# Performance work log

Hardware: AMD Instinct MI355X
Metric: run time of the kernel (lower is better)

## Reference

```python
import jax, jax.numpy as jnp
import numpy as np

NUM_NODES = 80000
NUM_EDGES = 1280000
NUM_GRAPHS = 512
IN_DIM = 64
HID = 64
NUM_CLASSES = 10


def setup_inputs() -> dict:
    key = jax.random.key(0)
    ks = jax.random.split(key, 16)
    x = jax.random.normal(ks[0], (NUM_NODES, IN_DIM), dtype=jnp.float32)
    edge_index = jax.random.randint(ks[1], (2, NUM_EDGES), 0, NUM_NODES, dtype=jnp.int64)
    batch = jnp.sort(jax.random.randint(ks[2], (NUM_NODES,), 0, NUM_GRAPHS, dtype=jnp.int64))

    def glorot(k, shape):
        fan_in, fan_out = shape[1], shape[0]
        lim = jnp.sqrt(6.0 / (fan_in + fan_out))
        return jax.random.uniform(k, shape, dtype=jnp.float32, minval=-lim, maxval=lim)

    inp = {
        "x": x,
        "edge_index": edge_index,
        "batch": batch,
        # GraphConv layer 1: lin_rel (with bias) applied to aggregated neighbors, lin_root (no bias)
        "w_rel1": glorot(ks[3], (HID, IN_DIM)),
        "b_rel1": jnp.zeros((HID,), dtype=jnp.float32),
        "w_root1": glorot(ks[4], (HID, IN_DIM)),
        # layer 2
        "w_rel2": glorot(ks[5], (HID, HID)),
        "b_rel2": jnp.zeros((HID,), dtype=jnp.float32),
        "w_root2": glorot(ks[6], (HID, HID)),
        # layer 3
        "w_rel3": glorot(ks[7], (HID, HID)),
        "b_rel3": jnp.zeros((HID,), dtype=jnp.float32),
        "w_root3": glorot(ks[8], (HID, HID)),
        # final linear head
        "w_lin": glorot(ks[9], (NUM_CLASSES, HID)),
        "b_lin": jnp.zeros((NUM_CLASSES,), dtype=jnp.float32),
    }
    return inp


def _graph_conv(x, src, dst, w_rel, b_rel, w_root):
    # PyG GraphConv with aggr='add': out_i = W_rel @ (sum_{j in N(i)} x_j) + b_rel + W_root @ x_i
    agg = jax.ops.segment_sum(x[src], dst, num_segments=NUM_NODES)  # [N, d_in]
    return agg @ w_rel.T + b_rel + x @ w_root.T


def reference(x, edge_index, batch,
              w_rel1, b_rel1, w_root1,
              w_rel2, b_rel2, w_root2,
              w_rel3, b_rel3, w_root3,
              w_lin, b_lin):
    src, dst = edge_index[0], edge_index[1]
    h = jax.nn.relu(_graph_conv(x, src, dst, w_rel1, b_rel1, w_root1))
    h = jax.nn.relu(_graph_conv(h, src, dst, w_rel2, b_rel2, w_root2))
    h = _graph_conv(h, src, dst, w_rel3, b_rel3, w_root3)
    # global_mean_pool over graph ids
    sums = jax.ops.segment_sum(h, batch, num_segments=NUM_GRAPHS)          # [G, HID]
    counts = jax.ops.segment_sum(jnp.ones((h.shape[0],), h.dtype), batch, num_segments=NUM_GRAPHS)
    pooled = sums / jnp.maximum(counts, 1.0)[:, None]
    # dropout p=0.5 is identity at inference (training=False)
    return pooled @ w_lin.T + b_lin  # [G, NUM_CLASSES]
```

## Files before the change

kernel.cpp:

```cpp
#include <hip/hip_runtime.h>

#define N_NODES  80000
#define N_EDGES  1280000
#define N_GRAPHS 512
#define DIM      64
#define NCLS     10

#define ETILE    8192
#define NTILE    157
#define NCB      157
#define CBPAD    160

typedef short short8f __attribute__((ext_vector_type(8)));
typedef float float4f __attribute__((ext_vector_type(4)));

static __device__ __forceinline__ unsigned short f2bf(float f) {
    unsigned u = __float_as_uint(f);
    unsigned r = (u + 0x7FFFu + ((u >> 16) & 1u)) >> 16;
    return (unsigned short)r;
}
static __device__ __forceinline__ float bf_lo(unsigned v) { return __uint_as_float(v << 16); }
static __device__ __forceinline__ float bf_hi(unsigned v) { return __uint_as_float(v & 0xFFFF0000u); }

__global__ __launch_bounds__(256) void k_hist(const int* __restrict__ ei,
                                              int* __restrict__ hmat) {
    __shared__ int hist[NCB];
    int tile = blockIdx.x, t = threadIdx.x;
    for (int i = t; i < NCB; i += 256) hist[i] = 0;
    __syncthreads();
    int base = tile * ETILE;
    int end = base + ETILE; if (end > N_EDGES) end = N_EDGES;
    for (int i = base + t; i < end; i += 256)
        atomicAdd(&hist[ei[N_EDGES + i] >> 9], 1);
    __syncthreads();
    for (int i = t; i < NCB; i += 256) hmat[tile * CBPAD + i] = hist[i];
}

__global__ __launch_bounds__(256) void k_scanT(const int* __restrict__ hmat,
        int* __restrict__ obase, int* __restrict__ btot) {
    __shared__ int sa[256], sb[256];
    int b = blockIdx.x, t = threadIdx.x;
    int v = (t < NTILE) ? hmat[t * CBPAD + b] : 0;
    sa[t] = v; __syncthreads();
    int* sp = sa; int* dp = sb;
    for (int off = 1; off < 256; off <<= 1) {
        dp[t] = sp[t] + ((t >= off) ? sp[t - off] : 0);
        __syncthreads();
        int* tmp = sp; sp = dp; dp = tmp;
    }
    int incl = sp[t];
    if (t < NTILE) obase[t * CBPAD + b] = incl - v;
    if (t == NTILE - 1) btot[b] = incl;
}

__global__ __launch_bounds__(256) void k_scanB(const int* __restrict__ btot,
        int* __restrict__ bucketbase, int* __restrict__ rowptr) {
    __shared__ int sa[256], sb[256];
    int t = threadIdx.x;
    int v = (t < NCB) ? btot[t] : 0;
    sa[t] = v; __syncthreads();
    int* sp = sa; int* dp = sb;
    for (int off = 1; off < 256; off <<= 1) {
        dp[t] = sp[t] + ((t >= off) ? sp[t - off] : 0);
        __syncthreads();
        int* tmp = sp; sp = dp; dp = tmp;
    }
    int incl = sp[t];
    if (t < NCB) bucketbase[t] = incl - v;
    if (t == 0) { bucketbase[NCB] = N_EDGES; rowptr[N_NODES] = N_EDGES; }
}

__global__ __launch_bounds__(256) void k_scatter(const int* __restrict__ ei,
        const int* __restrict__ obase, const int* __restrict__ bucketbase,
        int* __restrict__ ebuf) {
    __shared__ int cur[NCB];
    int tile = blockIdx.x, t = threadIdx.x;
    for (int i = t; i < NCB; i += 256)
        cur[i] = bucketbase[i] + obase[tile * CBPAD + i];
    __syncthreads();
    int base = tile * ETILE;
    int end = base + ETILE; if (end > N_EDGES) end = N_EDGES;
    for (int i = base + t; i < end; i += 256) {
        int s = ei[i], d = ei[N_EDGES + i];
        int p = atomicAdd(&cur[d >> 9], 1);
        ebuf[p] = s | ((d & 511) << 17);
    }
}

__global__ __launch_bounds__(256) void k_csr(const int* __restrict__ ebuf,
        const int* __restrict__ bucketbase, int* __restrict__ rowptr,
        int* __restrict__ col) {
    __shared__ int cnt[512];
    __shared__ int sa[512], sb[512];
    __shared__ int cur[512];
    int b = blockIdx.x, t = threadIdx.x;
    int s = bucketbase[b], e = bucketbase[b + 1];
    cnt[t] = 0; cnt[t + 256] = 0;
    __syncthreads();
    for (int i = s + t; i < e; i += 256) atomicAdd(&cnt[ebuf[i] >> 17], 1);
    __syncthreads();
    sa[t] = cnt[t]; sa[t + 256] = cnt[t + 256];
    __syncthreads();
    int* sp = sa; int* dp = sb;
    for (int off = 1; off < 512; off <<= 1) {
        int i1 = t + 256;
        int v0 = sp[t]  + ((t  >= off) ? sp[t  - off] : 0);
        int v1 = sp[i1] + ((i1 >= off) ? sp[i1 - off] : 0);
        __syncthreads();
        dp[t] = v0; dp[i1] = v1;
        __syncthreads();
        int* tmp = sp; sp = dp; dp = tmp;
    }
    int node0 = b * 512;
    int base0 = s + sp[t] - cnt[t];
    int base1 = s + sp[t + 256] - cnt[t + 256];
    cur[t] = base0; cur[t + 256] = base1;
    if (node0 + t < N_NODES)       rowptr[node0 + t] = base0;
    if (node0 + t + 256 < N_NODES) rowptr[node0 + t + 256] = base1;
    __syncthreads();
    for (int i = s + t; i < e; i += 256) {
        int pk = ebuf[i];
        int p = atomicAdd(&cur[pk >> 17], 1);
        col[p] = pk & 0x1FFFF;
    }
}

__global__ __launch_bounds__(256) void k_prep2(const float* __restrict__ x,
        const float* __restrict__ wr1, const float* __restrict__ wo1,
        const float* __restrict__ wr2, const float* __restrict__ wo2,
        unsigned short* __restrict__ xb, unsigned short* __restrict__ wf) {
    int bid = blockIdx.x, t = threadIdx.x;
    if (bid < 5000) {
        int i = bid * 256 + t;
        float4 v = ((const float4*)x)[i];
        ushort4 o;
        o.x = f2bf(v.x); o.y = f2bf(v.y); o.z = f2bf(v.z); o.w = f2bf(v.w);
        ((ushort4*)xb)[i] = o;
    } else {
        int idx = (bid - 5000) * 256 + t;
        int j = idx & 7, lane = (idx >> 3) & 63;
        int ks = (idx >> 9) & 3, nt = (idx >> 11) & 3, l = idx >> 13;
        int k = ks * 32 + ((lane >> 4) & 3) * 8 + j;
        int n = nt * 16 + (lane & 15);
        const float* wr = (l == 0) ? wr1 : wr2;
        const float* wo = (l == 0) ? wo1 : wo2;
        float val = (k < 64) ? wr[n * 64 + k] : wo[n * 64 + (k - 64)];
        wf[idx] = f2bf(val);
    }
}

__global__ __launch_bounds__(256) void k_gather_bf(const unsigned short* __restrict__ Xbf,
        const int* __restrict__ rowptr, const int* __restrict__ col,
        unsigned short* __restrict__ agg) {
    const unsigned* Xu = (const unsigned*)Xbf;
    int t = threadIdx.x, w = t >> 6, lane = t & 63;
    int g = lane >> 5, c = lane & 31;
    int node = blockIdx.x * 8 + w * 2 + g;
    int start = rowptr[node], end = rowptr[node + 1];
    float alo = 0.f, ahi = 0.f;
    int e = start;
    for (; e + 16 <= end; e += 16) {
        unsigned v[16];
#pragma unroll
        for (int j = 0; j < 16; ++j)
            v[j] = Xu[(size_t)col[e + j] * 32 + c];
#pragma unroll
        for (int j = 0; j < 16; ++j) { alo += bf_lo(v[j]); ahi += bf_hi(v[j]); }
    }
    for (; e + 4 <= end; e += 4) {
        unsigned v0 = Xu[(size_t)col[e]     * 32 + c];
        unsigned v1 = Xu[(size_t)col[e + 1] * 32 + c];
        unsigned v2 = Xu[(size_t)col[e + 2] * 32 + c];
        unsigned v3 = Xu[(size_t)col[e + 3] * 32 + c];
        alo += (bf_lo(v0) + bf_lo(v1)) + (bf_lo(v2) + bf_lo(v3));
        ahi += (bf_hi(v0) + bf_hi(v1)) + (bf_hi(v2) + bf_hi(v3));
    }
    for (; e < end; ++e) {
        unsigned v = Xu[(size_t)col[e] * 32 + c];
        alo += bf_lo(v); ahi += bf_hi(v);
    }
    unsigned o = (unsigned)f2bf(alo) | ((unsigned)f2bf(ahi) << 16);
    ((unsigned*)agg)[(size_t)node * 32 + c] = o;
}

__global__ __launch_bounds__(256) void k_linear_mfma(
        const unsigned short* __restrict__ aggb, const unsigned short* __restrict__ xb,
        const unsigned short* __restrict__ wf, const float* __restrict__ bias,
        unsigned short* __restrict__ out, int relu) {
    int t = threadIdx.x, w = t >> 6, lane = t & 63;
    int quad = lane >> 4, l15 = lane & 15;
    int mbase = blockIdx.x * 64 + w * 16;
    size_t arow = (size_t)(mbase + l15) * 64;
    short8f a0 = *(const short8f*)(aggb + arow + quad * 8);
    short8f a1 = *(const short8f*)(aggb + arow + 32 + quad * 8);
    short8f a2 = *(const short8f*)(xb   + arow + quad * 8);
    short8f a3 = *(const short8f*)(xb   + arow + 32 + quad * 8);
    int orow = mbase + quad * 4;
#pragma unroll
    for (int nt = 0; nt < 4; ++nt) {
        const unsigned short* wp = wf + ((size_t)(nt * 4) * 64 + lane) * 8;
        short8f b0 = *(const short8f*)(wp);
        short8f b1 = *(const short8f*)(wp + 64 * 8);
        short8f b2 = *(const short8f*)(wp + 128 * 8);
        short8f b3 = *(const short8f*)(wp + 192 * 8);
        float4f acc = {0.f, 0.f, 0.f, 0.f};
        acc = __builtin_amdgcn_mfma_f32_16x16x32_bf16(a0, b0, acc, 0, 0, 0);
        acc = __builtin_amdgcn_mfma_f32_16x16x32_bf16(a1, b1, acc, 0, 0, 0);
        acc = __builtin_amdgcn_mfma_f32_16x16x32_bf16(a2, b2, acc, 0, 0, 0);
        acc = __builtin_amdgcn_mfma_f32_16x16x32_bf16(a3, b3, acc, 0, 0, 0);
        float bi = bias[nt * 16 + l15];
#pragma unroll
        for (int r = 0; r < 4; ++r) {
            float v = acc[r] + bi;
            if (relu) v = fmaxf(v, 0.f);
            out[(size_t)(orow + r) * 64 + nt * 16 + l15] = f2bf(v);
        }
    }
}

static __device__ __forceinline__ int lowerb(const int* a, int n, int key) {
    int lo = 0, hi = n;
    while (lo < hi) { int mid = (lo + hi) >> 1; if (a[mid] < key) lo = mid + 1; else hi = mid; }
    return lo;
}

__global__ __launch_bounds__(256) void k_gsum(const unsigned short* __restrict__ h2,
        const int* __restrict__ rowptr, const int* __restrict__ col,
        const int* __restrict__ batch, float* __restrict__ S) {
    __shared__ float red1[8][64];
    __shared__ float red2[8][64];
    const unsigned* Xu = (const unsigned*)h2;
    int g = blockIdx.x, t = threadIdx.x;
    int hw = t >> 5, c = t & 31;
    int ns = lowerb(batch, N_NODES, g);
    int ne = lowerb(batch, N_NODES, g + 1);
    int es = rowptr[ns], ee = rowptr[ne];
    float alo = 0.f, ahi = 0.f;
    int nfull = (ee - es) >> 7;
    int e0 = es + hw * 16;
    for (int b = 0; b < nfull; ++b, e0 += 128) {
        unsigned v[16];
#pragma unroll
        for (int j = 0; j < 16; ++j)
            v[j] = Xu[(size_t)col[e0 + j] * 32 + c];
#pragma unroll
        for (int j = 0; j < 16; ++j) { alo += bf_lo(v[j]); ahi += bf_hi(v[j]); }
    }
    for (int e = es + nfull * 128 + hw; e < ee; e += 8) {
        unsigned v = Xu[(size_t)col[e] * 32 + c];
        alo += bf_lo(v); ahi += bf_hi(v);
    }
    float blo = 0.f, bhi = 0.f;
    for (int i = ns + hw; i < ne; i += 8) {
        unsigned v = Xu[(size_t)i * 32 + c];
        blo += bf_lo(v); bhi += bf_hi(v);
    }
    red1[hw][2 * c] = alo; red1[hw][2 * c + 1] = ahi;
    red2[hw][2 * c] = blo; red2[hw][2 * c + 1] = bhi;
    __syncthreads();
    if (t < 64) {
        float v = 0.f;
#pragma unroll
        for (int s = 0; s < 8; ++s) v += red1[s][t];
        S[g * 128 + t] = v;
    } else if (t < 128) {
        float v = 0.f;
#pragma unroll
        for (int s = 0; s < 8; ++s) v += red2[s][t - 64];
        S[g * 128 + 64 + (t - 64)] = v;
    }
}

__global__ __launch_bounds__(64) void k_head2(const float* __restrict__ S,
        const int* __restrict__ batch,
        const float* __restrict__ wr3, const float* __restrict__ wo3,
        const float* __restrict__ b3,
        const float* __restrict__ wlin, const float* __restrict__ blin,
        float* __restrict__ out) {
    __shared__ float s1[64], s2[64], pl[64];
    int g = blockIdx.x, t = threadIdx.x;
    int ns = lowerb(batch, N_NODES, g);
    int ne = lowerb(batch, N_NODES, g + 1);
    float inv = 1.f / (float)((ne > ns) ? (ne - ns) : 1);
    s1[t] = S[g * 128 + t] * inv;
    s2[t] = S[g * 128 + 64 + t] * inv;
    __syncthreads();
    float acc = b3[t];
    for (int k = 0; k < 64; ++k)
        acc += s1[k] * wr3[t * 64 + k] + s2[k] * wo3[t * 64 + k];
    pl[t] = acc;
    __syncthreads();
    float myout = 0.f;
    for (int cls = 0; cls < NCLS; ++cls) {
        float vv = pl[t] * wlin[cls * 64 + t];
        for (int off = 32; off > 0; off >>= 1) vv += __shfl_xor(vv, off);
        if (t == cls) myout = vv + blin[cls];
    }
    if (t < NCLS) out[g * NCLS + t] = myout;
}

extern "C" void kernel_launch(void* const* d_in, const int* in_sizes, int n_in,
                              void* d_out, int out_size, void* d_ws, size_t ws_size,
                              hipStream_t stream) {
    const float* x     = (const float*)d_in[0];
    const int*   ei    = (const int*)d_in[1];
    const int*   batch = (const int*)d_in[2];
    const float* wr1 = (const float*)d_in[3];
    const float* b1  = (const float*)d_in[4];
    const float* wo1 = (const float*)d_in[5];
    const float* wr2 = (const float*)d_in[6];
    const float* b2  = (const float*)d_in[7];
    const float* wo2 = (const float*)d_in[8];
    const float* wr3 = (const float*)d_in[9];
    const float* b3  = (const float*)d_in[10];
    const float* wo3 = (const float*)d_in[11];
    const float* wlin = (const float*)d_in[12];
    const float* blin = (const float*)d_in[13];
    float* out = (float*)d_out;

    char* p = (char*)d_ws;
    auto alloc = [&](size_t bytes) { char* r = p; p += (bytes + 255) & ~(size_t)255; return r; };
    int*   rowptr  = (int*)alloc((N_NODES + 1) * sizeof(int));
    int*   hmat    = (int*)alloc((size_t)NTILE * CBPAD * sizeof(int));
    int*   obase   = (int*)alloc((size_t)NTILE * CBPAD * sizeof(int));
    int*   btot    = (int*)alloc(CBPAD * sizeof(int));
    int*   bucketbase = (int*)alloc((NCB + 1) * sizeof(int));
    int*   ebuf    = (int*)alloc((size_t)N_EDGES * sizeof(int));
    int*   col     = (int*)alloc((size_t)N_EDGES * sizeof(int));
    unsigned short* wf  = (unsigned short*)alloc(2 * 8192 * sizeof(unsigned short));
    unsigned short* xbf = (unsigned short*)alloc((size_t)N_NODES * 64 * 2);
    unsigned short* agg = (unsigned short*)alloc((size_t)N_NODES * 64 * 2);
    unsigned short* hA  = (unsigned short*)alloc((size_t)N_NODES * 64 * 2);
    unsigned short* hB  = (unsigned short*)alloc((size_t)N_NODES * 64 * 2);
    float* S       = (float*)alloc((size_t)N_GRAPHS * 128 * sizeof(float));

    k_hist   <<<NTILE, 256, 0, stream>>>(ei, hmat);
    k_scanT  <<<NCB,   256, 0, stream>>>(hmat, obase, btot);
    k_scanB  <<<1,     256, 0, stream>>>(btot, bucketbase, rowptr);
    k_scatter<<<NTILE, 256, 0, stream>>>(ei, obase, bucketbase, ebuf);
    k_csr    <<<NCB,   256, 0, stream>>>(ebuf, bucketbase, rowptr, col);
    k_prep2  <<<5064,  256, 0, stream>>>(x, wr1, wo1, wr2, wo2, xbf, wf);

    k_gather_bf  <<<N_NODES / 8,  256, 0, stream>>>(xbf, rowptr, col, agg);
    k_linear_mfma<<<N_NODES / 64, 256, 0, stream>>>(agg, xbf, wf,        b1, hA, 1);
    k_gather_bf  <<<N_NODES / 8,  256, 0, stream>>>(hA, rowptr, col, agg);
    k_linear_mfma<<<N_NODES / 64, 256, 0, stream>>>(agg, hA, wf + 8192,  b2, hB, 1);
    k_gsum <<<N_GRAPHS, 256, 0, stream>>>(hB, rowptr, col, batch, S);
    k_head2<<<N_GRAPHS, 64,  0, stream>>>(S, batch, wr3, wo3, b3, wlin, blin, out);
}
```

Before: 279.9 us.

## Gather rows with 16-byte loads across edges and split graph sums four ways

The neighbour gather now has one wavefront per node, with eight lanes per edge each loading 16 bytes, so eight edges are in flight per step. Partial sums are then reduced with cross-lane shuffles, in place of the old scheme where each half-wave streamed all edges with 4-byte loads. The graph-sum kernel splits each graph's node range into four blocks, raising block count for better occupancy, and the head kernel adds the four partials. The cost is extra shuffle work and idle lanes on low-degree nodes.

```diff
diff --git a/kernel.cpp b/kernel.cpp
--- a/kernel.cpp
+++ b/kernel.cpp
@@ -149,38 +149,56 @@
     }
 }
 
-__global__ __launch_bounds__(256) void k_gather_bf(const unsigned short* __restrict__ Xbf,
+__global__ __launch_bounds__(256) void k_gather4(const unsigned short* __restrict__ Xbf,
         const int* __restrict__ rowptr, const int* __restrict__ col,
         unsigned short* __restrict__ agg) {
-    const unsigned* Xu = (const unsigned*)Xbf;
+    const uint4* Xq = (const uint4*)Xbf;
     int t = threadIdx.x, w = t >> 6, lane = t & 63;
-    int g = lane >> 5, c = lane & 31;
-    int node = blockIdx.x * 8 + w * 2 + g;
+    int e = lane >> 3, c = lane & 7;
+    int node = blockIdx.x * 4 + w;
     int start = rowptr[node], end = rowptr[node + 1];
-    float alo = 0.f, ahi = 0.f;
-    int e = start;
-    for (; e + 16 <= end; e += 16) {
-        unsigned v[16];
-#pragma unroll
-        for (int j = 0; j < 16; ++j)
-            v[j] = Xu[(size_t)col[e + j] * 32 + c];
-#pragma unroll
-        for (int j = 0; j < 16; ++j) { alo += bf_lo(v[j]); ahi += bf_hi(v[j]); }
-    }
-    for (; e + 4 <= end; e += 4) {
-        unsigned v0 = Xu[(size_t)col[e]     * 32 + c];
-        unsigned v1 = Xu[(size_t)col[e + 1] * 32 + c];
-        unsigned v2 = Xu[(size_t)col[e + 2] * 32 + c];
-        unsigned v3 = Xu[(size_t)col[e + 3] * 32 + c];
-        alo += (bf_lo(v0) + bf_lo(v1)) + (bf_lo(v2) + bf_lo(v3));
-        ahi += (bf_hi(v0) + bf_hi(v1)) + (bf_hi(v2) + bf_hi(v3));
-    }
-    for (; e < end; ++e) {
-        unsigned v = Xu[(size_t)col[e] * 32 + c];
-        alo += bf_lo(v); ahi += bf_hi(v);
-    }
-    unsigned o = (unsigned)f2bf(alo) | ((unsigned)f2bf(ahi) << 16);
-    ((unsigned*)agg)[(size_t)node * 32 + c] = o;
+    float acc[8] = {0.f, 0.f, 0.f, 0.f, 0.f, 0.f, 0.f, 0.f};
+    int base = start;
+    for (; base + 16 <= end; base += 16) {
+        int i0 = col[base + e];
+        int i1 = col[base + 8 + e];
+        uint4 v0 = Xq[(size_t)i0 * 8 + c];
+        uint4 v1 = Xq[(size_t)i1 * 8 + c];
+        acc[0] += bf_lo(v0.x) + bf_lo(v1.x); acc[1] += bf_hi(v0.x) + bf_hi(v1.x);
+        acc[2] += bf_lo(v0.y) + bf_lo(v1.y); acc[3] += bf_hi(v0.y) + bf_hi(v1.y);
+        acc[4] += bf_lo(v0.z) + bf_lo(v1.z); acc[5] += bf_hi(v0.z) + bf_hi(v1.z);
+        acc[6] += bf_lo(v0.w) + bf_lo(v1.w); acc[7] += bf_hi(v0.w) + bf_hi(v1.w);
+    }
+    for (; base + 8 <= end; base += 8) {
+        int i0 = col[base + e];
+        uint4 v0 = Xq[(size_t)i0 * 8 + c];
+        acc[0] += bf_lo(v0.x); acc[1] += bf_hi(v0.x);
+        acc[2] += bf_lo(v0.y); acc[3] += bf_hi(v0.y);
+        acc[4] += bf_lo(v0.z); acc[5] += bf_hi(v0.z);
+        acc[6] += bf_lo(v0.w); acc[7] += bf_hi(v0.w);
+    }
+    int r = end - base;
+    if (e < r) {
+        int i0 = col[base + e];
+        uint4 v0 = Xq[(size_t)i0 * 8 + c];
+        acc[0] += bf_lo(v0.x); acc[1] += bf_hi(v0.x);
+        acc[2] += bf_lo(v0.y); acc[3] += bf_hi(v0.y);
+        acc[4] += bf_lo(v0.z); acc[5] += bf_hi(v0.z);
+        acc[6] += bf_lo(v0.w); acc[7] += bf_hi(v0.w);
+    }
+#pragma unroll
+    for (int off = 8; off < 64; off <<= 1) {
+#pragma unroll
+        for (int j = 0; j < 8; ++j) acc[j] += __shfl_xor(acc[j], off);
+    }
+    if (e == 0) {
+        uint4 o;
+        o.x = (unsigned)f2bf(acc[0]) | ((unsigned)f2bf(acc[1]) << 16);
+        o.y = (unsigned)f2bf(acc[2]) | ((unsigned)f2bf(acc[3]) << 16);
+        o.z = (unsigned)f2bf(acc[4]) | ((unsigned)f2bf(acc[5]) << 16);
+        o.w = (unsigned)f2bf(acc[6]) | ((unsigned)f2bf(acc[7]) << 16);
+        ((uint4*)agg)[(size_t)node * 8 + c] = o;
+    }
 }
 
 __global__ __launch_bounds__(256) void k_linear_mfma(
@@ -226,15 +244,18 @@
 
 __global__ __launch_bounds__(256) void k_gsum(const unsigned short* __restrict__ h2,
         const int* __restrict__ rowptr, const int* __restrict__ col,
-        const int* __restrict__ batch, float* __restrict__ S) {
+        const int* __restrict__ batch, float* __restrict__ S4) {
     __shared__ float red1[8][64];
     __shared__ float red2[8][64];
     const unsigned* Xu = (const unsigned*)h2;
-    int g = blockIdx.x, t = threadIdx.x;
+    int g = blockIdx.x >> 2, part = blockIdx.x & 3;
+    int t = threadIdx.x;
     int hw = t >> 5, c = t & 31;
     int ns = lowerb(batch, N_NODES, g);
     int ne = lowerb(batch, N_NODES, g + 1);
-    int es = rowptr[ns], ee = rowptr[ne];
+    int a0 = ns + (int)(((long long)(ne - ns) * part) >> 2);
+    int a1 = ns + (int)(((long long)(ne - ns) * (part + 1)) >> 2);
+    int es = rowptr[a0], ee = rowptr[a1];
     float alo = 0.f, ahi = 0.f;
     int nfull = (ee - es) >> 7;
     int e0 = es + hw * 16;
@@ -251,7 +272,7 @@
         alo += bf_lo(v); ahi += bf_hi(v);
     }
     float blo = 0.f, bhi = 0.f;
-    for (int i = ns + hw; i < ne; i += 8) {
+    for (int i = a0 + hw; i < a1; i += 8) {
         unsigned v = Xu[(size_t)i * 32 + c];
         blo += bf_lo(v); bhi += bf_hi(v);
     }
@@ -262,16 +283,16 @@
         float v = 0.f;
 #pragma unroll
         for (int s = 0; s < 8; ++s) v += red1[s][t];
-        S[g * 128 + t] = v;
+        S4[(size_t)blockIdx.x * 128 + t] = v;
     } else if (t < 128) {
         float v = 0.f;
 #pragma unroll
         for (int s = 0; s < 8; ++s) v += red2[s][t - 64];
-        S[g * 128 + 64 + (t - 64)] = v;
-    }
-}
-
-__global__ __launch_bounds__(64) void k_head2(const float* __restrict__ S,
+        S4[(size_t)blockIdx.x * 128 + 64 + (t - 64)] = v;
+    }
+}
+
+__global__ __launch_bounds__(64) void k_head2(const float* __restrict__ S4,
         const int* __restrict__ batch,
         const float* __restrict__ wr3, const float* __restrict__ wo3,
         const float* __restrict__ b3,
@@ -282,8 +303,9 @@
     int ns = lowerb(batch, N_NODES, g);
     int ne = lowerb(batch, N_NODES, g + 1);
     float inv = 1.f / (float)((ne > ns) ? (ne - ns) : 1);
-    s1[t] = S[g * 128 + t] * inv;
-    s2[t] = S[g * 128 + 64 + t] * inv;
+    const float* Sg = S4 + (size_t)g * 4 * 128;
+    s1[t] = (Sg[t]       + Sg[128 + t]       + Sg[256 + t]       + Sg[384 + t]) * inv;
+    s2[t] = (Sg[64 + t]  + Sg[192 + t]       + Sg[320 + t]       + Sg[448 + t]) * inv;
     __syncthreads();
     float acc = b3[t];
     for (int k = 0; k < 64; ++k)
@@ -332,7 +354,7 @@
     unsigned short* agg = (unsigned short*)alloc((size_t)N_NODES * 64 * 2);
     unsigned short* hA  = (unsigned short*)alloc((size_t)N_NODES * 64 * 2);
     unsigned short* hB  = (unsigned short*)alloc((size_t)N_NODES * 64 * 2);
-    float* S       = (float*)alloc((size_t)N_GRAPHS * 128 * sizeof(float));
+    float* S4      = (float*)alloc((size_t)N_GRAPHS * 4 * 128 * sizeof(float));
 
     k_hist   <<<NTILE, 256, 0, stream>>>(ei, hmat);
     k_scanT  <<<NCB,   256, 0, stream>>>(hmat, obase, btot);
@@ -341,10 +363,10 @@
     k_csr    <<<NCB,   256, 0, stream>>>(ebuf, bucketbase, rowptr, col);
     k_prep2  <<<5064,  256, 0, stream>>>(x, wr1, wo1, wr2, wo2, xbf, wf);
 
-    k_gather_bf  <<<N_NODES / 8,  256, 0, stream>>>(xbf, rowptr, col, agg);
+    k_gather4    <<<N_NODES / 4,  256, 0, stream>>>(xbf, rowptr, col, agg);
     k_linear_mfma<<<N_NODES / 64, 256, 0, stream>>>(agg, xbf, wf,        b1, hA, 1);
-    k_gather_bf  <<<N_NODES / 8,  256, 0, stream>>>(hA, rowptr, col, agg);
+    k_gather4    <<<N_NODES / 4,  256, 0, stream>>>(hA, rowptr, col, agg);
     k_linear_mfma<<<N_NODES / 64, 256, 0, stream>>>(agg, hA, wf + 8192,  b2, hB, 1);
-    k_gsum <<<N_GRAPHS, 256, 0, stream>>>(hB, rowptr, col, batch, S);
-    k_head2<<<N_GRAPHS, 64,  0, stream>>>(S, batch, wr3, wo3, b3, wlin, blin, out);
-}
+    k_gsum <<<N_GRAPHS * 4, 256, 0, stream>>>(hB, rowptr, col, batch, S4);
+    k_head2<<<N_GRAPHS,     64,  0, stream>>>(S4, batch, wr3, wo3, b3, wlin, blin, out);
+}
```

Result: faster. 266.1 us (-4.9%).
